# Optimization experiments

Measured on AMD Instinct MI355X. Metric: run time of the kernel, lower is better.

## Reference

```python
import jax, jax.numpy as jnp
import numpy as np

N, IN_F, OUT_F, H = 2048, 512, 256, 4
NH = OUT_F // H  # n_hidden per head (is_concat=True)
NEG_SLOPE = 0.2
NEG_INF = -1e9  # finite stand-in for -inf in masked softmax


def setup_inputs() -> dict:
    key = jax.random.key(0)
    k1, k2, k3, k4, k5 = jax.random.split(key, 5)
    h = jax.random.normal(k1, (N, IN_F), dtype=jnp.float32)
    adj = jax.random.randint(k2, (N, N), 0, 2).astype(jnp.float32)
    adj = jnp.maximum(adj, jnp.eye(N, dtype=jnp.float32))  # self-loops -> no empty rows
    adj_mat = adj[:, :, None]  # [N, N, 1]
    s = jax.random.uniform(k3, (N, N, 1), dtype=jnp.float32)
    W_lin = jax.random.normal(k4, (IN_F, H * NH), dtype=jnp.float32) / np.sqrt(IN_F)
    attn_w = jax.random.normal(k5, (2 * NH,), dtype=jnp.float32) / np.sqrt(2 * NH)
    return {"h": h, "adj_mat": adj_mat, "s": s, "W_lin": W_lin, "attn_w": attn_w}


def reference(h, adj_mat, s, W_lin, attn_w):
    n = h.shape[0]
    g = (h @ W_lin).reshape(n, H, NH)  # [N, H, nh]
    # attn(Linear(2*nh,1)) on cat(g_i, g_j) == a_src.g_i + a_dst.g_j
    a_src, a_dst = attn_w[:NH], attn_w[NH:]
    el = jnp.einsum('nhf,f->nh', g, a_src)  # source (row i) term
    er = jnp.einsum('nhf,f->nh', g, a_dst)  # dest   (col j) term
    e = jax.nn.leaky_relu(el[:, None, :] + er[None, :, :], NEG_SLOPE)  # [N, N, H]
    mask = adj_mat == 0  # [N, N, 1] broadcasts over heads
    e = jnp.where(mask, NEG_INF, e)
    s_m = jnp.where(mask, NEG_INF, s)  # [N, N, 1]
    a = jax.nn.softmax(e, axis=1)
    s_prime = jax.nn.softmax(s_m, axis=1)
    new_attention = jax.nn.softmax(a + s_prime, axis=1)  # [N, N, H] (dropout=identity, eval)
    attn_res = jnp.einsum('ijh,jhf->ihf', new_attention, g)  # [N, H, nh]
    return attn_res.reshape(n, H * NH)
```

## Files before the change

kernel.cpp:

```cpp
#include <hip/hip_runtime.h>

#define NN 2048
#define KK 512

typedef __attribute__((ext_vector_type(8))) short bf16x8;
typedef __attribute__((ext_vector_type(4))) float f32x4;

__device__ inline ushort f2bf(float x) {
  union { float f; unsigned u; } v; v.f = x;
  unsigned r = v.u + 0x7fffu + ((v.u >> 16) & 1u);
  return (ushort)(r >> 16);
}

__global__ __launch_bounds__(256) void k_gemm(
    const float* __restrict__ hin, const float* __restrict__ W,
    const float* __restrict__ aw, float* __restrict__ g,
    float* __restrict__ el, float* __restrict__ er) {
  __shared__ float hs[4][512];
  const int tid = threadIdx.x;
  const int r0 = blockIdx.x * 4;

  const float4* hsrc = (const float4*)(hin + r0 * 512);
  float4* hdst = (float4*)&hs[0][0];
  hdst[tid] = hsrc[tid];
  hdst[tid + 256] = hsrc[tid + 256];
  __syncthreads();

  float acc[4] = {0.f, 0.f, 0.f, 0.f};
#pragma unroll 8
  for (int k = 0; k < 512; ++k) {
    float wk = W[k * 256 + tid];
#pragma unroll
    for (int r = 0; r < 4; ++r) acc[r] += hs[r][k] * wk;
  }
#pragma unroll
  for (int r = 0; r < 4; ++r) g[(r0 + r) * 256 + tid] = acc[r];

  const int lane = tid & 63;
  const int w = tid >> 6;
  const float asrc = aw[lane];
  const float adst = aw[64 + lane];
#pragma unroll
  for (int r = 0; r < 4; ++r) {
    float e1 = acc[r] * asrc;
    float e2 = acc[r] * adst;
#pragma unroll
    for (int m = 1; m < 64; m <<= 1) {
      e1 += __shfl_xor(e1, m);
      e2 += __shfl_xor(e2, m);
    }
    if (lane == 0) {
      el[(r0 + r) * 4 + w] = e1;
      er[(r0 + r) * 4 + w] = e2;
    }
  }
}

__global__ __launch_bounds__(256) void k_prep(
    const float* __restrict__ g, const float* __restrict__ el,
    const float* __restrict__ er, ushort* __restrict__ gTb,
    float* __restrict__ Eel, float* __restrict__ Fel,
    float* __restrict__ Eer_jh, float* __restrict__ Fer_jh,
    float* __restrict__ Eer_hj, float* __restrict__ Fer_hj) {
  const int bx = blockIdx.x;
  const int t = threadIdx.x;
  if (bx < 128) {
    __shared__ float ts[64][65];
    const int r0 = (bx >> 2) * 64;
    const int c0 = (bx & 3) * 64;
    const int tr = t >> 6;
    const int tc = t & 63;
#pragma unroll
    for (int i = 0; i < 16; ++i)
      ts[tr + i * 4][tc] = g[(size_t)(r0 + tr + i * 4) * 256 + c0 + tc];
    __syncthreads();
#pragma unroll
    for (int i = 0; i < 16; ++i) {
      float v = ts[tc][tr + i * 4];
      const int j = r0 + tc;
      const int f = c0 + tr + i * 4;
      gTb[(size_t)(j >> 3) * 2048 + f * 8 + (j & 7)] = f2bf(v);
    }
  } else {
    const int idx = (bx - 128) * 256 + t;
    float4 e4 = *(const float4*)(el + idx * 4);
    float4 r4 = *(const float4*)(er + idx * 4);
    float el_[4] = {e4.x, e4.y, e4.z, e4.w};
    float er_[4] = {r4.x, r4.y, r4.z, r4.w};
    float eel[4], fel[4], eer[4], fer[4];
#pragma unroll
    for (int h = 0; h < 4; ++h) {
      eel[h] = __expf(el_[h]);
      fel[h] = __expf(0.2f * el_[h]);
      eer[h] = __expf(er_[h]);
      fer[h] = __expf(0.2f * er_[h]);
    }
    *(float4*)(Eel + idx * 4) = make_float4(eel[0], eel[1], eel[2], eel[3]);
    *(float4*)(Fel + idx * 4) = make_float4(fel[0], fel[1], fel[2], fel[3]);
    *(float4*)(Eer_jh + idx * 4) = make_float4(eer[0], eer[1], eer[2], eer[3]);
    *(float4*)(Fer_jh + idx * 4) = make_float4(fer[0], fer[1], fer[2], fer[3]);
#pragma unroll
    for (int h = 0; h < 4; ++h) {
      Eer_hj[h * NN + idx] = eer[h];
      Fer_hj[h * NN + idx] = fer[h];
    }
  }
}

__global__ __launch_bounds__(256) void k_rowz(
    const float* __restrict__ adj, const float* __restrict__ s,
    const float* __restrict__ Eel, const float* __restrict__ Fel,
    const float* __restrict__ Eer_jh, const float* __restrict__ Fer_jh,
    float* __restrict__ rZ1, float* __restrict__ rZ2,
    unsigned long long* __restrict__ maskb) {
  const int row = blockIdx.x;
  const int tid = threadIdx.x;
  const int wq = tid >> 6;
  const int lane = tid & 63;

  float4 e4 = *(const float4*)(Eel + row * 4);
  float4 f4 = *(const float4*)(Fel + row * 4);
  const float eel[4] = {e4.x, e4.y, e4.z, e4.w};
  const float fel[4] = {f4.x, f4.y, f4.z, f4.w};

  float z1[4] = {0.f, 0.f, 0.f, 0.f};
  float z2 = 0.f;

  const float* ap = adj + (size_t)row * NN + wq * 512;
  const float* sp = s + (size_t)row * NN + wq * 512;

#pragma unroll
  for (int it = 0; it < 8; ++it) {
    const int j = it * 64 + lane;
    float a = ap[j];
    float sv = sp[j];
    bool nb = (a != 0.f);
    unsigned long long m = __ballot(nb);
    if (lane == 0) maskb[row * 32 + wq * 8 + it] = m;
    const int jg = wq * 512 + j;
    float4 eer4 = *(const float4*)(Eer_jh + jg * 4);
    float4 fer4 = *(const float4*)(Fer_jh + jg * 4);
    z2 += nb ? __expf(sv) : 0.f;
    float ev[4] = {eer4.x, eer4.y, eer4.z, eer4.w};
    float fv[4] = {fer4.x, fer4.y, fer4.z, fer4.w};
#pragma unroll
    for (int h = 0; h < 4; ++h) {
      float p = eel[h] * ev[h];
      float q = fel[h] * fv[h];
      float E = (p > 1.f) ? p : q;
      z1[h] += nb ? E : 0.f;
    }
  }

#pragma unroll
  for (int m = 1; m < 64; m <<= 1) {
    z2 += __shfl_xor(z2, m);
#pragma unroll
    for (int h = 0; h < 4; ++h) z1[h] += __shfl_xor(z1[h], m);
  }

  __shared__ float wr[4][5];
  if (lane == 0) {
    wr[wq][0] = z1[0]; wr[wq][1] = z1[1]; wr[wq][2] = z1[2]; wr[wq][3] = z1[3];
    wr[wq][4] = z2;
  }
  __syncthreads();
  if (tid < 5) {
    float sum = wr[0][tid] + wr[1][tid] + wr[2][tid] + wr[3][tid];
    if (tid < 4) rZ1[row * 4 + tid] = 1.f / sum;
    else rZ2[row] = 1.f / sum;
  }
}

__global__ __launch_bounds__(256, 8) void k_attn(
    const float* __restrict__ s, const unsigned long long* __restrict__ maskb,
    const ushort* __restrict__ gTb,
    const float* __restrict__ Eel, const float* __restrict__ Fel,
    const float* __restrict__ Eer_hj, const float* __restrict__ Fer_hj,
    const float* __restrict__ rZ1, const float* __restrict__ rZ2,
    _Float16* __restrict__ U, float* __restrict__ Z3p) {
  const int tid = threadIdx.x;
  const int h = tid >> 6;
  const int lane = tid & 63;
  const int il = lane & 15;
  const int kg = lane >> 4;
  const int ib = blockIdx.x >> 4;
  const int jc = blockIdx.x & 15;
  const int i0 = ib * 16;
  const int jb0 = jc * 128;
  const int row = i0 + il;

  const float eel = Eel[row * 4 + h];
  const float fel = Fel[row * 4 + h];
  const float rz1 = rZ1[row * 4 + h];
  const float rz2 = rZ2[row];

  const unsigned long long* mp = maskb + row * 32 + jc * 2;
  const unsigned long long m0 = mp[0];
  const unsigned long long m1 = mp[1];

  f32x4 acc[4];
#pragma unroll
  for (int nt = 0; nt < 4; ++nt) acc[nt] = (f32x4){0.f, 0.f, 0.f, 0.f};
  float z3 = 0.f;

  const float* sp = s + (size_t)row * NN + jb0 + kg * 8;
  const float* eerp = Eer_hj + h * NN + jb0 + kg * 8;
  const float* ferp = Fer_hj + h * NN + jb0 + kg * 8;
  const ushort* bp = gTb + (size_t)(jc * 16 + kg) * 2048 + (h * 64 + il) * 8;

#pragma unroll
  for (int ks = 0; ks < 4; ++ks) {
    const int o = ks * 32;
    unsigned long long w = (ks & 2) ? m1 : m0;
    unsigned byte_ = (unsigned)(w >> ((ks & 1) * 32 + kg * 8)) & 0xffu;

    bf16x8 A;
#pragma unroll
    for (int gp = 0; gp < 2; ++gp) {
      float4 s4 = *(const float4*)(sp + o + gp * 4);
      float4 ee4 = *(const float4*)(eerp + o + gp * 4);
      float4 fe4 = *(const float4*)(ferp + o + gp * 4);
      float sv[4] = {s4.x, s4.y, s4.z, s4.w};
      float ev[4] = {ee4.x, ee4.y, ee4.z, ee4.w};
      float fv[4] = {fe4.x, fe4.y, fe4.z, fe4.w};
#pragma unroll
      for (int e = 0; e < 4; ++e) {
        bool nb = (byte_ >> (gp * 4 + e)) & 1u;
        float spv = __expf(sv[e]) * rz2;
        float p = eel * ev[e];
        float q = fel * fv[e];
        float E = (p > 1.f) ? p : q;
        float tt = nb ? (E * rz1 + spv) : 0.f;
        float c = __expf(tt);
        z3 += c;
        A[gp * 4 + e] = (short)f2bf(c);
      }
    }

    const ushort* bks = bp + (size_t)(ks * 4) * 2048;
    acc[0] = __builtin_amdgcn_mfma_f32_16x16x32_bf16(A, *(const bf16x8*)(bks), acc[0], 0, 0, 0);
    acc[1] = __builtin_amdgcn_mfma_f32_16x16x32_bf16(A, *(const bf16x8*)(bks + 128), acc[1], 0, 0, 0);
    acc[2] = __builtin_amdgcn_mfma_f32_16x16x32_bf16(A, *(const bf16x8*)(bks + 256), acc[2], 0, 0, 0);
    acc[3] = __builtin_amdgcn_mfma_f32_16x16x32_bf16(A, *(const bf16x8*)(bks + 384), acc[3], 0, 0, 0);
  }

  z3 += __shfl_xor(z3, 16);
  z3 += __shfl_xor(z3, 32);
  if (lane < 16)
    Z3p[jc * (NN * 4) + (i0 + lane) * 4 + h] = z3;

  _Float16* up = U + (size_t)jc * (NN * 256) + (size_t)i0 * 256 + h * 64 + il;
#pragma unroll
  for (int nt = 0; nt < 4; ++nt)
#pragma unroll
    for (int q = 0; q < 4; ++q)
      up[(size_t)(kg * 4 + q) * 256 + nt * 16] = (_Float16)acc[nt][q];
}

__global__ __launch_bounds__(256) void k_final(
    const _Float16* __restrict__ U, const float* __restrict__ Z3p,
    float* __restrict__ out) {
  const int i = blockIdx.x;
  const int c = threadIdx.x;
  const int h = c >> 6;
  float u = 0.f, z = 0.f;
#pragma unroll
  for (int p = 0; p < 16; ++p) {
    u += (float)U[(size_t)p * (NN * 256) + (size_t)i * 256 + c];
    z += Z3p[p * (NN * 4) + i * 4 + h];
  }
  out[(size_t)i * 256 + c] = u / z;
}

extern "C" void kernel_launch(void* const* d_in, const int* in_sizes, int n_in,
                              void* d_out, int out_size, void* d_ws, size_t ws_size,
                              hipStream_t stream) {
  const float* hin = (const float*)d_in[0];
  const float* adj = (const float*)d_in[1];
  const float* s = (const float*)d_in[2];
  const float* W = (const float*)d_in[3];
  const float* aw = (const float*)d_in[4];
  float* out = (float*)d_out;

  float* ws = (float*)d_ws;
  _Float16* U   = (_Float16*)ws;
  float* g      = ws;
  float* el     = ws + 4194304;
  float* er     = ws + 4202496;
  float* Eel    = ws + 4210688;
  float* Fel    = ws + 4218880;
  float* Eer_jh = ws + 4227072;
  float* Fer_jh = ws + 4235264;
  float* Eer_hj = ws + 4243456;
  float* Fer_hj = ws + 4251648;
  float* rZ1    = ws + 4259840;
  float* rZ2    = ws + 4268032;
  float* Z3p    = ws + 4270080;
  unsigned long long* maskb = (unsigned long long*)(ws + 4401152);
  ushort* gTb   = (ushort*)(ws + 4532224);

  k_gemm<<<512, 256, 0, stream>>>(hin, W, aw, g, el, er);
  k_prep<<<136, 256, 0, stream>>>(g, el, er, gTb, Eel, Fel, Eer_jh, Fer_jh, Eer_hj, Fer_hj);
  k_rowz<<<2048, 256, 0, stream>>>(adj, s, Eel, Fel, Eer_jh, Fer_jh, rZ1, rZ2, maskb);
  k_attn<<<2048, 256, 0, stream>>>(s, maskb, gTb, Eel, Fel, Eer_hj, Fer_hj, rZ1, rZ2, U, Z3p);
  k_final<<<2048, 256, 0, stream>>>(U, Z3p, out);
}
```

Measured before the change: 69.60 us.

## Split-K the projection GEMM, separate table prep, and halve attention column splits

The projection GEMM now tiles 16 rows per block and splits K into four partial slabs. Each W load is reused across 16 rows, and the partials are summed later in the transpose and exp-table kernels, which are now separate launches. The attention kernel covers 256 columns per block instead of 128, so it launches half as many blocks and the final reduction reads 8 partials instead of 16. This trades extra partial-sum traffic and an additional launch for better W reuse and less partial-output traffic from the attention stage.

```diff
diff --git a/kernel.cpp b/kernel.cpp
--- a/kernel.cpp
+++ b/kernel.cpp
@@ -14,34 +14,45 @@
 
 __global__ __launch_bounds__(256) void k_gemm(
     const float* __restrict__ hin, const float* __restrict__ W,
-    const float* __restrict__ aw, float* __restrict__ g,
-    float* __restrict__ el, float* __restrict__ er) {
-  __shared__ float hs[4][512];
+    const float* __restrict__ aw, float* __restrict__ gp,
+    float* __restrict__ elp, float* __restrict__ erp) {
+  __shared__ float hs[16][132];
   const int tid = threadIdx.x;
-  const int r0 = blockIdx.x * 4;
-
-  const float4* hsrc = (const float4*)(hin + r0 * 512);
-  float4* hdst = (float4*)&hs[0][0];
-  hdst[tid] = hsrc[tid];
-  hdst[tid + 256] = hsrc[tid + 256];
+  const int ib = blockIdx.x >> 2;
+  const int kh = blockIdx.x & 3;
+  const int i0 = ib * 16;
+  const int k0 = kh * 128;
+
+#pragma unroll
+  for (int p = 0; p < 2; ++p) {
+    int idx = tid + p * 256;
+    int row = idx >> 5;
+    int c4 = (idx & 31) << 2;
+    *(float4*)&hs[row][c4] = *(const float4*)(hin + (size_t)(i0 + row) * KK + k0 + c4);
+  }
   __syncthreads();
 
-  float acc[4] = {0.f, 0.f, 0.f, 0.f};
-#pragma unroll 8
-  for (int k = 0; k < 512; ++k) {
-    float wk = W[k * 256 + tid];
-#pragma unroll
-    for (int r = 0; r < 4; ++r) acc[r] += hs[r][k] * wk;
-  }
-#pragma unroll
-  for (int r = 0; r < 4; ++r) g[(r0 + r) * 256 + tid] = acc[r];
+  float acc[16];
+#pragma unroll
+  for (int r = 0; r < 16; ++r) acc[r] = 0.f;
+
+#pragma unroll 4
+  for (int k = 0; k < 128; ++k) {
+    float wk = W[(size_t)(k0 + k) * 256 + tid];
+#pragma unroll
+    for (int r = 0; r < 16; ++r) acc[r] += hs[r][k] * wk;
+  }
+
+  float* go = gp + (size_t)kh * (NN * 256);
+#pragma unroll
+  for (int r = 0; r < 16; ++r) go[(size_t)(i0 + r) * 256 + tid] = acc[r];
 
   const int lane = tid & 63;
   const int w = tid >> 6;
   const float asrc = aw[lane];
   const float adst = aw[64 + lane];
 #pragma unroll
-  for (int r = 0; r < 4; ++r) {
+  for (int r = 0; r < 16; ++r) {
     float e1 = acc[r] * asrc;
     float e2 = acc[r] * adst;
 #pragma unroll
@@ -50,60 +61,69 @@
       e2 += __shfl_xor(e2, m);
     }
     if (lane == 0) {
-      el[(r0 + r) * 4 + w] = e1;
-      er[(r0 + r) * 4 + w] = e2;
+      elp[kh * 8192 + (i0 + r) * 4 + w] = e1;
+      erp[kh * 8192 + (i0 + r) * 4 + w] = e2;
     }
   }
 }
 
-__global__ __launch_bounds__(256) void k_prep(
-    const float* __restrict__ g, const float* __restrict__ el,
-    const float* __restrict__ er, ushort* __restrict__ gTb,
+__global__ __launch_bounds__(256) void k_tables(
+    const float* __restrict__ elp, const float* __restrict__ erp,
     float* __restrict__ Eel, float* __restrict__ Fel,
     float* __restrict__ Eer_jh, float* __restrict__ Fer_jh,
     float* __restrict__ Eer_hj, float* __restrict__ Fer_hj) {
+  const int idx = blockIdx.x * 256 + threadIdx.x;
+  float el_[4] = {0.f, 0.f, 0.f, 0.f};
+  float er_[4] = {0.f, 0.f, 0.f, 0.f};
+#pragma unroll
+  for (int kh = 0; kh < 4; ++kh) {
+    float4 e4 = *(const float4*)(elp + kh * 8192 + idx * 4);
+    float4 r4 = *(const float4*)(erp + kh * 8192 + idx * 4);
+    el_[0] += e4.x; el_[1] += e4.y; el_[2] += e4.z; el_[3] += e4.w;
+    er_[0] += r4.x; er_[1] += r4.y; er_[2] += r4.z; er_[3] += r4.w;
+  }
+  float eel[4], fel[4], eer[4], fer[4];
+#pragma unroll
+  for (int h = 0; h < 4; ++h) {
+    eel[h] = __expf(el_[h]);
+    fel[h] = __expf(0.2f * el_[h]);
+    eer[h] = __expf(er_[h]);
+    fer[h] = __expf(0.2f * er_[h]);
+  }
+  *(float4*)(Eel + idx * 4) = make_float4(eel[0], eel[1], eel[2], eel[3]);
+  *(float4*)(Fel + idx * 4) = make_float4(fel[0], fel[1], fel[2], fel[3]);
+  *(float4*)(Eer_jh + idx * 4) = make_float4(eer[0], eer[1], eer[2], eer[3]);
+  *(float4*)(Fer_jh + idx * 4) = make_float4(fer[0], fer[1], fer[2], fer[3]);
+#pragma unroll
+  for (int h = 0; h < 4; ++h) {
+    Eer_hj[h * NN + idx] = eer[h];
+    Fer_hj[h * NN + idx] = fer[h];
+  }
+}
+
+__global__ __launch_bounds__(256) void k_prep(
+    const float* __restrict__ gp, ushort* __restrict__ gTb) {
+  __shared__ float ts[64][65];
   const int bx = blockIdx.x;
   const int t = threadIdx.x;
-  if (bx < 128) {
-    __shared__ float ts[64][65];
-    const int r0 = (bx >> 2) * 64;
-    const int c0 = (bx & 3) * 64;
-    const int tr = t >> 6;
-    const int tc = t & 63;
-#pragma unroll
-    for (int i = 0; i < 16; ++i)
-      ts[tr + i * 4][tc] = g[(size_t)(r0 + tr + i * 4) * 256 + c0 + tc];
-    __syncthreads();
-#pragma unroll
-    for (int i = 0; i < 16; ++i) {
-      float v = ts[tc][tr + i * 4];
-      const int j = r0 + tc;
-      const int f = c0 + tr + i * 4;
-      gTb[(size_t)(j >> 3) * 2048 + f * 8 + (j & 7)] = f2bf(v);
-    }
-  } else {
-    const int idx = (bx - 128) * 256 + t;
-    float4 e4 = *(const float4*)(el + idx * 4);
-    float4 r4 = *(const float4*)(er + idx * 4);
-    float el_[4] = {e4.x, e4.y, e4.z, e4.w};
-    float er_[4] = {r4.x, r4.y, r4.z, r4.w};
-    float eel[4], fel[4], eer[4], fer[4];
-#pragma unroll
-    for (int h = 0; h < 4; ++h) {
-      eel[h] = __expf(el_[h]);
-      fel[h] = __expf(0.2f * el_[h]);
-      eer[h] = __expf(er_[h]);
-      fer[h] = __expf(0.2f * er_[h]);
-    }
-    *(float4*)(Eel + idx * 4) = make_float4(eel[0], eel[1], eel[2], eel[3]);
-    *(float4*)(Fel + idx * 4) = make_float4(fel[0], fel[1], fel[2], fel[3]);
-    *(float4*)(Eer_jh + idx * 4) = make_float4(eer[0], eer[1], eer[2], eer[3]);
-    *(float4*)(Fer_jh + idx * 4) = make_float4(fer[0], fer[1], fer[2], fer[3]);
-#pragma unroll
-    for (int h = 0; h < 4; ++h) {
-      Eer_hj[h * NN + idx] = eer[h];
-      Fer_hj[h * NN + idx] = fer[h];
-    }
+  const int r0 = (bx >> 2) * 64;
+  const int c0 = (bx & 3) * 64;
+  const int tr = t >> 6;
+  const int tc = t & 63;
+#pragma unroll
+  for (int i = 0; i < 16; ++i) {
+    size_t off = (size_t)(r0 + tr + i * 4) * 256 + c0 + tc;
+    float v = gp[off] + gp[off + (size_t)(NN * 256)] +
+              gp[off + (size_t)(2 * NN * 256)] + gp[off + (size_t)(3 * NN * 256)];
+    ts[tr + i * 4][tc] = v;
+  }
+  __syncthreads();
+#pragma unroll
+  for (int i = 0; i < 16; ++i) {
+    float v = ts[tc][tr + i * 4];
+    const int j = r0 + tc;
+    const int f = c0 + tr + i * 4;
+    gTb[(size_t)(j >> 3) * 2048 + f * 8 + (j & 7)] = f2bf(v);
   }
 }
 
@@ -184,10 +204,10 @@
   const int lane = tid & 63;
   const int il = lane & 15;
   const int kg = lane >> 4;
-  const int ib = blockIdx.x >> 4;
-  const int jc = blockIdx.x & 15;
+  const int ib = blockIdx.x >> 3;
+  const int jc = blockIdx.x & 7;
   const int i0 = ib * 16;
-  const int jb0 = jc * 128;
+  const int jb0 = jc * 256;
   const int row = i0 + il;
 
   const float eel = Eel[row * 4 + h];
@@ -195,9 +215,11 @@
   const float rz1 = rZ1[row * 4 + h];
   const float rz2 = rZ2[row];
 
-  const unsigned long long* mp = maskb + row * 32 + jc * 2;
+  const unsigned long long* mp = maskb + row * 32 + jc * 4;
   const unsigned long long m0 = mp[0];
   const unsigned long long m1 = mp[1];
+  const unsigned long long m2 = mp[2];
+  const unsigned long long m3 = mp[3];
 
   f32x4 acc[4];
 #pragma unroll
@@ -207,12 +229,14 @@
   const float* sp = s + (size_t)row * NN + jb0 + kg * 8;
   const float* eerp = Eer_hj + h * NN + jb0 + kg * 8;
   const float* ferp = Fer_hj + h * NN + jb0 + kg * 8;
-  const ushort* bp = gTb + (size_t)(jc * 16 + kg) * 2048 + (h * 64 + il) * 8;
-
-#pragma unroll
-  for (int ks = 0; ks < 4; ++ks) {
+  const ushort* bp = gTb + (size_t)(jc * 32 + kg) * 2048 + (h * 64 + il) * 8;
+
+#pragma unroll
+  for (int ks = 0; ks < 8; ++ks) {
     const int o = ks * 32;
-    unsigned long long w = (ks & 2) ? m1 : m0;
+    unsigned long long w = (ks >> 1) == 0 ? m0
+                         : (ks >> 1) == 1 ? m1
+                         : (ks >> 1) == 2 ? m2 : m3;
     unsigned byte_ = (unsigned)(w >> ((ks & 1) * 32 + kg * 8)) & 0xffu;
 
     bf16x8 A;
@@ -266,7 +290,7 @@
   const int h = c >> 6;
   float u = 0.f, z = 0.f;
 #pragma unroll
-  for (int p = 0; p < 16; ++p) {
+  for (int p = 0; p < 8; ++p) {
     u += (float)U[(size_t)p * (NN * 256) + (size_t)i * 256 + c];
     z += Z3p[p * (NN * 4) + i * 4 + h];
   }
@@ -284,25 +308,26 @@
   float* out = (float*)d_out;
 
   float* ws = (float*)d_ws;
-  _Float16* U   = (_Float16*)ws;
-  float* g      = ws;
-  float* el     = ws + 4194304;
-  float* er     = ws + 4202496;
-  float* Eel    = ws + 4210688;
-  float* Fel    = ws + 4218880;
-  float* Eer_jh = ws + 4227072;
-  float* Fer_jh = ws + 4235264;
-  float* Eer_hj = ws + 4243456;
-  float* Fer_hj = ws + 4251648;
-  float* rZ1    = ws + 4259840;
-  float* rZ2    = ws + 4268032;
-  float* Z3p    = ws + 4270080;
-  unsigned long long* maskb = (unsigned long long*)(ws + 4401152);
-  ushort* gTb   = (ushort*)(ws + 4532224);
-
-  k_gemm<<<512, 256, 0, stream>>>(hin, W, aw, g, el, er);
-  k_prep<<<136, 256, 0, stream>>>(g, el, er, gTb, Eel, Fel, Eer_jh, Fer_jh, Eer_hj, Fer_hj);
+  float* gp     = ws;
+  float* elp    = ws + 2097152;
+  float* erp    = ws + 2129920;
+  float* Eel    = ws + 2162688;
+  float* Fel    = ws + 2170880;
+  float* Eer_jh = ws + 2179072;
+  float* Fer_jh = ws + 2187264;
+  float* Eer_hj = ws + 2195456;
+  float* Fer_hj = ws + 2203648;
+  float* rZ1    = ws + 2211840;
+  float* rZ2    = ws + 2220032;
+  float* Z3p    = ws + 2222080;
+  unsigned long long* maskb = (unsigned long long*)(ws + 2287616);
+  ushort* gTb   = (ushort*)(ws + 2418688);
+  _Float16* U   = (_Float16*)(ws + 2680832);
+
+  k_gemm<<<512, 256, 0, stream>>>(hin, W, aw, gp, elp, erp);
+  k_tables<<<8, 256, 0, stream>>>(elp, erp, Eel, Fel, Eer_jh, Fer_jh, Eer_hj, Fer_hj);
+  k_prep<<<128, 256, 0, stream>>>(gp, gTb);
   k_rowz<<<2048, 256, 0, stream>>>(adj, s, Eel, Fel, Eer_jh, Fer_jh, rZ1, rZ2, maskb);
-  k_attn<<<2048, 256, 0, stream>>>(s, maskb, gTb, Eel, Fel, Eer_hj, Fer_hj, rZ1, rZ2, U, Z3p);
+  k_attn<<<1024, 256, 0, stream>>>(s, maskb, gTb, Eel, Fel, Eer_hj, Fer_hj, rZ1, rZ2, U, Z3p);
   k_final<<<2048, 256, 0, stream>>>(U, Z3p, out);
 }
```

After: 72.37 us. 1.04x slower.

## Move feature GEMM to split-bf16 MFMA and write transposed gTb directly

Applied to the files above, without the earlier changes.

Replaces the scalar FP32 h@W GEMM with a bf16 MFMA GEMM. It keeps near-FP32 accuracy by splitting h and W into hi/lo bf16 parts (three MFMAs per tile), with a new small kernel that pre-splits and transposes W each call. The GEMM epilogue writes the bf16 interleaved gTb layout and el/er directly, which removes the separate transpose pass and the full FP32 g round-trip. It also swaps the leaky-relu selector for fmaxf and compacts the workspace layout. This adds one launch and two hi/lo product passes, so it trades more MFMA work for less global traffic.

```diff
diff --git a/kernel.cpp b/kernel.cpp
--- a/kernel.cpp
+++ b/kernel.cpp
@@ -12,98 +12,155 @@
   return (ushort)(r >> 16);
 }
 
+__global__ __launch_bounds__(256) void k_wprep(
+    const float* __restrict__ W, ushort* __restrict__ wthi,
+    ushort* __restrict__ wtlo) {
+  __shared__ float ts[64][65];
+  const int t = threadIdx.x;
+  const int kb = (blockIdx.x >> 2) * 64;
+  const int nb = (blockIdx.x & 3) * 64;
+  const int r = t >> 6, c = t & 63;
+#pragma unroll
+  for (int p = 0; p < 16; ++p)
+    ts[p * 4 + r][c] = W[(size_t)(kb + p * 4 + r) * 256 + nb + c];
+  __syncthreads();
+#pragma unroll
+  for (int p = 0; p < 16; ++p) {
+    int n = p * 4 + r;
+    int k = c;
+    float v = ts[k][n];
+    union { float f; unsigned u; } q; q.f = v;
+    ushort hi = (ushort)(q.u >> 16);
+    union { float f; unsigned u; } hf; hf.u = q.u & 0xffff0000u;
+    ushort lo = f2bf(v - hf.f);
+    size_t off = (size_t)(nb + n) * KK + kb + k;
+    wthi[off] = hi;
+    wtlo[off] = lo;
+  }
+}
+
 __global__ __launch_bounds__(256) void k_gemm(
-    const float* __restrict__ hin, const float* __restrict__ W,
-    const float* __restrict__ aw, float* __restrict__ g,
-    float* __restrict__ el, float* __restrict__ er) {
-  __shared__ float hs[4][512];
+    const float* __restrict__ hin, const ushort* __restrict__ wthi,
+    const ushort* __restrict__ wtlo, const float* __restrict__ aw,
+    ushort* __restrict__ gTb, float* __restrict__ el, float* __restrict__ er) {
+  __shared__ float hs[16][516];
   const int tid = threadIdx.x;
-  const int r0 = blockIdx.x * 4;
-
-  const float4* hsrc = (const float4*)(hin + r0 * 512);
-  float4* hdst = (float4*)&hs[0][0];
-  hdst[tid] = hsrc[tid];
-  hdst[tid + 256] = hsrc[tid + 256];
+  const int i0 = blockIdx.x * 16;
+#pragma unroll
+  for (int p = 0; p < 8; ++p) {
+    int g4 = tid + p * 256;
+    int row = g4 >> 7, col = (g4 & 127) << 2;
+    *(float4*)&hs[row][col] = *(const float4*)(hin + (size_t)(i0 + row) * KK + col);
+  }
   __syncthreads();
 
-  float acc[4] = {0.f, 0.f, 0.f, 0.f};
-#pragma unroll 8
-  for (int k = 0; k < 512; ++k) {
-    float wk = W[k * 256 + tid];
-#pragma unroll
-    for (int r = 0; r < 4; ++r) acc[r] += hs[r][k] * wk;
-  }
-#pragma unroll
-  for (int r = 0; r < 4; ++r) g[(r0 + r) * 256 + tid] = acc[r];
-
+  const int h = tid >> 6;
   const int lane = tid & 63;
-  const int w = tid >> 6;
-  const float asrc = aw[lane];
-  const float adst = aw[64 + lane];
-#pragma unroll
-  for (int r = 0; r < 4; ++r) {
-    float e1 = acc[r] * asrc;
-    float e2 = acc[r] * adst;
-#pragma unroll
-    for (int m = 1; m < 64; m <<= 1) {
-      e1 += __shfl_xor(e1, m);
-      e2 += __shfl_xor(e2, m);
-    }
-    if (lane == 0) {
-      el[(r0 + r) * 4 + w] = e1;
-      er[(r0 + r) * 4 + w] = e2;
-    }
-  }
-}
-
-__global__ __launch_bounds__(256) void k_prep(
-    const float* __restrict__ g, const float* __restrict__ el,
-    const float* __restrict__ er, ushort* __restrict__ gTb,
+  const int il = lane & 15;
+  const int kg = lane >> 4;
+
+  f32x4 acc[4];
+#pragma unroll
+  for (int nt = 0; nt < 4; ++nt) acc[nt] = (f32x4){0.f, 0.f, 0.f, 0.f};
+
+  const ushort* bh_base = wthi + (size_t)(h * 64 + il) * KK;
+  const ushort* bl_base = wtlo + (size_t)(h * 64 + il) * KK;
+
+#pragma unroll 4
+  for (int ks = 0; ks < 16; ++ks) {
+    const int ko = ks * 32 + kg * 8;
+    float4 a01 = *(const float4*)&hs[il][ko];
+    float4 a23 = *(const float4*)&hs[il][ko + 4];
+    float av[8] = {a01.x, a01.y, a01.z, a01.w, a23.x, a23.y, a23.z, a23.w};
+    union { unsigned u[4]; bf16x8 v; } Ah, Al;
+#pragma unroll
+    for (int p = 0; p < 4; ++p) {
+      union { float f; unsigned u; } u0, u1;
+      u0.f = av[2 * p]; u1.f = av[2 * p + 1];
+      Ah.u[p] = (u0.u >> 16) | (u1.u & 0xffff0000u);
+      union { float f; unsigned u; } h0, h1;
+      h0.u = u0.u & 0xffff0000u;
+      h1.u = u1.u & 0xffff0000u;
+      union { float f; unsigned u; } r0, r1;
+      r0.f = av[2 * p] - h0.f;
+      r1.f = av[2 * p + 1] - h1.f;
+      Al.u[p] = (r0.u >> 16) | (r1.u & 0xffff0000u);
+    }
+#pragma unroll
+    for (int nt = 0; nt < 4; ++nt) {
+      bf16x8 Bh = *(const bf16x8*)(bh_base + nt * 16 * KK + ko);
+      bf16x8 Bl = *(const bf16x8*)(bl_base + nt * 16 * KK + ko);
+      acc[nt] = __builtin_amdgcn_mfma_f32_16x16x32_bf16(Ah.v, Bh, acc[nt], 0, 0, 0);
+      acc[nt] = __builtin_amdgcn_mfma_f32_16x16x32_bf16(Al.v, Bh, acc[nt], 0, 0, 0);
+      acc[nt] = __builtin_amdgcn_mfma_f32_16x16x32_bf16(Ah.v, Bl, acc[nt], 0, 0, 0);
+    }
+  }
+
+  const int jb = (i0 >> 3) + (kg >> 1);
+  const int halfoff = (kg & 1) * 4;
+#pragma unroll
+  for (int nt = 0; nt < 4; ++nt) {
+    const int f = h * 64 + nt * 16 + il;
+    unsigned w0 = (unsigned)f2bf(acc[nt][0]) | ((unsigned)f2bf(acc[nt][1]) << 16);
+    unsigned w1 = (unsigned)f2bf(acc[nt][2]) | ((unsigned)f2bf(acc[nt][3]) << 16);
+    uint2 pk = make_uint2(w0, w1);
+    *(uint2*)(gTb + (size_t)jb * 2048 + f * 8 + halfoff) = pk;
+  }
+
+  float ela[4] = {0.f, 0.f, 0.f, 0.f}, era[4] = {0.f, 0.f, 0.f, 0.f};
+#pragma unroll
+  for (int nt = 0; nt < 4; ++nt) {
+    float as = aw[nt * 16 + il];
+    float ad = aw[64 + nt * 16 + il];
+#pragma unroll
+    for (int q = 0; q < 4; ++q) {
+      ela[q] += acc[nt][q] * as;
+      era[q] += acc[nt][q] * ad;
+    }
+  }
+#pragma unroll
+  for (int m = 1; m < 16; m <<= 1) {
+#pragma unroll
+    for (int q = 0; q < 4; ++q) {
+      ela[q] += __shfl_xor(ela[q], m);
+      era[q] += __shfl_xor(era[q], m);
+    }
+  }
+  if (il == 0) {
+#pragma unroll
+    for (int q = 0; q < 4; ++q) {
+      el[(i0 + kg * 4 + q) * 4 + h] = ela[q];
+      er[(i0 + kg * 4 + q) * 4 + h] = era[q];
+    }
+  }
+}
+
+__global__ __launch_bounds__(256) void k_tables(
+    const float* __restrict__ el, const float* __restrict__ er,
     float* __restrict__ Eel, float* __restrict__ Fel,
     float* __restrict__ Eer_jh, float* __restrict__ Fer_jh,
     float* __restrict__ Eer_hj, float* __restrict__ Fer_hj) {
-  const int bx = blockIdx.x;
-  const int t = threadIdx.x;
-  if (bx < 128) {
-    __shared__ float ts[64][65];
-    const int r0 = (bx >> 2) * 64;
-    const int c0 = (bx & 3) * 64;
-    const int tr = t >> 6;
-    const int tc = t & 63;
-#pragma unroll
-    for (int i = 0; i < 16; ++i)
-      ts[tr + i * 4][tc] = g[(size_t)(r0 + tr + i * 4) * 256 + c0 + tc];
-    __syncthreads();
-#pragma unroll
-    for (int i = 0; i < 16; ++i) {
-      float v = ts[tc][tr + i * 4];
-      const int j = r0 + tc;
-      const int f = c0 + tr + i * 4;
-      gTb[(size_t)(j >> 3) * 2048 + f * 8 + (j & 7)] = f2bf(v);
-    }
-  } else {
-    const int idx = (bx - 128) * 256 + t;
-    float4 e4 = *(const float4*)(el + idx * 4);
-    float4 r4 = *(const float4*)(er + idx * 4);
-    float el_[4] = {e4.x, e4.y, e4.z, e4.w};
-    float er_[4] = {r4.x, r4.y, r4.z, r4.w};
-    float eel[4], fel[4], eer[4], fer[4];
-#pragma unroll
-    for (int h = 0; h < 4; ++h) {
-      eel[h] = __expf(el_[h]);
-      fel[h] = __expf(0.2f * el_[h]);
-      eer[h] = __expf(er_[h]);
-      fer[h] = __expf(0.2f * er_[h]);
-    }
-    *(float4*)(Eel + idx * 4) = make_float4(eel[0], eel[1], eel[2], eel[3]);
-    *(float4*)(Fel + idx * 4) = make_float4(fel[0], fel[1], fel[2], fel[3]);
-    *(float4*)(Eer_jh + idx * 4) = make_float4(eer[0], eer[1], eer[2], eer[3]);
-    *(float4*)(Fer_jh + idx * 4) = make_float4(fer[0], fer[1], fer[2], fer[3]);
-#pragma unroll
-    for (int h = 0; h < 4; ++h) {
-      Eer_hj[h * NN + idx] = eer[h];
-      Fer_hj[h * NN + idx] = fer[h];
-    }
+  const int idx = blockIdx.x * 256 + threadIdx.x;
+  float4 e4 = *(const float4*)(el + idx * 4);
+  float4 r4 = *(const float4*)(er + idx * 4);
+  float el_[4] = {e4.x, e4.y, e4.z, e4.w};
+  float er_[4] = {r4.x, r4.y, r4.z, r4.w};
+  float eel[4], fel[4], eer[4], fer[4];
+#pragma unroll
+  for (int h = 0; h < 4; ++h) {
+    eel[h] = __expf(el_[h]);
+    fel[h] = __expf(0.2f * el_[h]);
+    eer[h] = __expf(er_[h]);
+    fer[h] = __expf(0.2f * er_[h]);
+  }
+  *(float4*)(Eel + idx * 4) = make_float4(eel[0], eel[1], eel[2], eel[3]);
+  *(float4*)(Fel + idx * 4) = make_float4(fel[0], fel[1], fel[2], fel[3]);
+  *(float4*)(Eer_jh + idx * 4) = make_float4(eer[0], eer[1], eer[2], eer[3]);
+  *(float4*)(Fer_jh + idx * 4) = make_float4(fer[0], fer[1], fer[2], fer[3]);
+#pragma unroll
+  for (int h = 0; h < 4; ++h) {
+    Eer_hj[h * NN + idx] = eer[h];
+    Fer_hj[h * NN + idx] = fer[h];
   }
 }
 
@@ -147,7 +204,7 @@
     for (int h = 0; h < 4; ++h) {
       float p = eel[h] * ev[h];
       float q = fel[h] * fv[h];
-      float E = (p > 1.f) ? p : q;
+      float E = fmaxf(p, q);
       z1[h] += nb ? E : 0.f;
     }
   }
@@ -230,7 +287,7 @@
         float spv = __expf(sv[e]) * rz2;
         float p = eel * ev[e];
         float q = fel * fv[e];
-        float E = (p > 1.f) ? p : q;
+        float E = fmaxf(p, q);
         float tt = nb ? (E * rz1 + spv) : 0.f;
         float c = __expf(tt);
         z3 += c;
@@ -284,24 +341,26 @@
   float* out = (float*)d_out;
 
   float* ws = (float*)d_ws;
-  _Float16* U   = (_Float16*)ws;
-  float* g      = ws;
-  float* el     = ws + 4194304;
-  float* er     = ws + 4202496;
-  float* Eel    = ws + 4210688;
-  float* Fel    = ws + 4218880;
-  float* Eer_jh = ws + 4227072;
-  float* Fer_jh = ws + 4235264;
-  float* Eer_hj = ws + 4243456;
-  float* Fer_hj = ws + 4251648;
-  float* rZ1    = ws + 4259840;
-  float* rZ2    = ws + 4268032;
-  float* Z3p    = ws + 4270080;
-  unsigned long long* maskb = (unsigned long long*)(ws + 4401152);
-  ushort* gTb   = (ushort*)(ws + 4532224);
-
-  k_gemm<<<512, 256, 0, stream>>>(hin, W, aw, g, el, er);
-  k_prep<<<136, 256, 0, stream>>>(g, el, er, gTb, Eel, Fel, Eer_jh, Fer_jh, Eer_hj, Fer_hj);
+  float* el     = ws;
+  float* er     = ws + 8192;
+  float* Eel    = ws + 16384;
+  float* Fel    = ws + 24576;
+  float* Eer_jh = ws + 32768;
+  float* Fer_jh = ws + 40960;
+  float* Eer_hj = ws + 49152;
+  float* Fer_hj = ws + 57344;
+  float* rZ1    = ws + 65536;
+  float* rZ2    = ws + 73728;
+  float* Z3p    = ws + 75776;
+  unsigned long long* maskb = (unsigned long long*)(ws + 206848);
+  ushort* wthi  = (ushort*)(ws + 337920);
+  ushort* wtlo  = (ushort*)(ws + 403456);
+  ushort* gTb   = (ushort*)(ws + 468992);
+  _Float16* U   = (_Float16*)(ws + 731136);
+
+  k_wprep<<<32, 256, 0, stream>>>(W, wthi, wtlo);
+  k_gemm<<<128, 256, 0, stream>>>(hin, wthi, wtlo, aw, gTb, el, er);
+  k_tables<<<8, 256, 0, stream>>>(el, er, Eel, Fel, Eer_jh, Fer_jh, Eer_hj, Fer_hj);
   k_rowz<<<2048, 256, 0, stream>>>(adj, s, Eel, Fel, Eer_jh, Fer_jh, rZ1, rZ2, maskb);
   k_attn<<<2048, 256, 0, stream>>>(s, maskb, gTb, Eel, Fel, Eer_hj, Fer_hj, rZ1, rZ2, U, Z3p);
   k_final<<<2048, 256, 0, stream>>>(U, Z3p, out);
```

After: 75.26 us. +8.1%, slower.
